# Kernel tuning notes

Measured on AMD Instinct MI355X. Metric: run time of the kernel, lower is better.

## Reference

```python
import jax, jax.numpy as jnp
import numpy as np

KERNEL_SIZE = 3
PADDING = KERNEL_SIZE // 2
EPS = 1e-12  # matches torch F.normalize default eps


def setup_inputs() -> dict:
    key = jax.random.key(0)
    k1, k2 = jax.random.split(key)
    query_feat = jax.random.normal(k1, (8, 512, 64, 64), dtype=jnp.float32)
    memory_bank = jax.random.normal(k2, (32, 512, 64, 64), dtype=jnp.float32)
    return {"query_feat": query_feat, "memory_bank": memory_bank}


def _l2_normalize(x, axis):
    n = jnp.sqrt(jnp.sum(x * x, axis=axis, keepdims=True))
    return x / jnp.maximum(n, EPS)


def reference(query_feat, memory_bank):
    # query_feat: (B, C, H, W); memory_bank: (M, C, H, W)
    b, c, h, w = query_feat.shape
    qn = _l2_normalize(query_feat, axis=1)
    mn = _l2_normalize(memory_bank, axis=1)
    # zero-pad memory spatially (matches F.unfold zero padding)
    mp = jnp.pad(mn, ((0, 0), (0, 0), (PADDING, PADDING), (PADDING, PADDING)))
    # Correlation via shifted dot-products over the K^2 window offsets,
    # keeping a running max instead of materializing (M, C, K^2, H, W).
    sim_max = None
    for di in range(KERNEL_SIZE):
        for dj in range(KERNEL_SIZE):
            shifted = mp[:, :, di:di + h, dj:dj + w]  # (M, C, H, W)
            s = jnp.einsum('mchw,bchw->bmhw', shifted, qn)  # cosine sims
            sim_max = s if sim_max is None else jnp.maximum(sim_max, s)
    pairwise = jnp.maximum(sim_max, 0.0)          # clamp(min=0), (B, M, H, W)
    group = jnp.mean(pairwise, axis=1)            # mean aggregation over M
    anomaly_map = 1.0 - group[:, None, :, :]      # (B, 1, H, W)
    return anomaly_map
```

## Files before the change

kernel.cpp:

```cpp
#include <hip/hip_runtime.h>

#define B_ 8
#define M_ 32
#define C_ 512
#define H_ 64
#define W_ 64
#define HW 4096
#define NKT 16
#define KC 32
#define TW 4
#define TH 4
#define NPOS 16
#define PW 6
#define PH 6
#define NPM 36
#define HP 66
#define WP 66
#define HPWP (HP*WP)

typedef __attribute__((ext_vector_type(8))) short short8;
typedef __attribute__((ext_vector_type(4))) float float4v;

static __device__ __forceinline__ unsigned pk_bf16(float lo, float hi) {
    unsigned r;
    asm("v_cvt_pk_bf16_f32 %0, %1, %2" : "=v"(r) : "v"(lo), "v"(hi));
    return r;
}

static __device__ __forceinline__ void load_lds16(const short* g, short* l) {
    __builtin_amdgcn_global_load_lds((const __attribute__((address_space(1))) void*)g,
                                     (__attribute__((address_space(3))) void*)l, 16, 0, 0);
}

__global__ void zero_norms(float* __restrict__ p) {
    int i = blockIdx.x * 256 + threadIdx.x;
    ((float4v*)p)[i] = (float4v){0.f, 0.f, 0.f, 0.f};
}

__global__ __launch_bounds__(512)
void prep_kernel(const float* __restrict__ Q, const float* __restrict__ Mb,
                 short* __restrict__ qT, short* __restrict__ mT,
                 float* __restrict__ nq, float* __restrict__ nm) {
    __shared__ unsigned buf[2][8704];

    const int tid = threadIdx.x;
    const bool isq = (blockIdx.x < 256);
    const int g  = isq ? (int)blockIdx.x : (int)blockIdx.x - 256;
    const int pr  = g >> 6;
    const int hq  = (g >> 2) & 15;
    const int ktg = g & 3;
    const float* base = (isq ? Q : Mb) + (size_t)(pr * 2) * C_ * HW;

    const int w4 = tid & 15, cpr = (tid >> 4) & 15, limg = tid >> 8;
    const float* lsrc = base + (size_t)limg * C_ * HW
                      + (size_t)(ktg * 128 + cpr * 2) * HW
                      + (size_t)(hq * 4) * W_ + w4 * 4;

    const int rw = tid & 63, rr2 = (tid >> 6) & 3, rim = tid >> 8;
    const unsigned* rb0 = &buf[0][(rr2 * 2 + rim) * 1088 + rw * 17];
    const unsigned* rb1 = &buf[1][(rr2 * 2 + rim) * 1088 + rw * 17];

    float4v s0 = {0.f,0.f,0.f,0.f}, s1 = s0, s2 = s0, s3 = s0;
    float4v A0, A1, A2, A3, B0, B1, B2, B3;

#define LOADP(ch) { const float* p_ = lsrc + (size_t)(ch) * 32 * HW; \
    A0 = *(const float4v*)(p_);       A1 = *(const float4v*)(p_ + 64); \
    A2 = *(const float4v*)(p_ + 128); A3 = *(const float4v*)(p_ + 192); \
    const float* q_ = p_ + HW; \
    B0 = *(const float4v*)(q_);       B1 = *(const float4v*)(q_ + 64); \
    B2 = *(const float4v*)(q_ + 128); B3 = *(const float4v*)(q_ + 192); }

#define WRITEP(bs) { unsigned* w_ = &buf[bs][limg * 1088 + cpr]; \
    s0 += A0 * A0 + B0 * B0; s1 += A1 * A1 + B1 * B1; \
    s2 += A2 * A2 + B2 * B2; s3 += A3 * A3 + B3 * B3; \
    _Pragma("unroll") \
    for (int j = 0; j < 4; ++j) { \
        w_[0 * 2176 + (w4 * 4 + j) * 17] = pk_bf16(A0[j], B0[j]); \
        w_[1 * 2176 + (w4 * 4 + j) * 17] = pk_bf16(A1[j], B1[j]); \
        w_[2 * 2176 + (w4 * 4 + j) * 17] = pk_bf16(A2[j], B2[j]); \
        w_[3 * 2176 + (w4 * 4 + j) * 17] = pk_bf16(A3[j], B3[j]); } }

#define STOREP(ch, rb) { union { unsigned u[16]; short8 v[4]; } o_; \
    _Pragma("unroll") \
    for (int q_i = 0; q_i < 16; ++q_i) o_.u[q_i] = (rb)[q_i]; \
    short* d_; \
    if (isq) d_ = qT + (((size_t)(ktg * 4 + (ch)) * HW + (size_t)(hq * 4 + rr2) * 64 + rw) * B_ \
                        + pr * 2 + rim) * KC; \
    else     d_ = mT + (((size_t)(ktg * 4 + (ch)) * HPWP + (size_t)(hq * 4 + rr2 + 1) * WP + rw + 1) * M_ \
                        + pr * 2 + rim) * KC; \
    *(short8*)(d_)      = o_.v[0]; *(short8*)(d_ + 8)  = o_.v[1]; \
    *(short8*)(d_ + 16) = o_.v[2]; *(short8*)(d_ + 24) = o_.v[3]; }

    LOADP(0); WRITEP(0); __syncthreads();
    LOADP(1); STOREP(0, rb0); WRITEP(1); __syncthreads();
    LOADP(2); STOREP(1, rb1); WRITEP(0); __syncthreads();
    LOADP(3); STOREP(2, rb0); WRITEP(1); __syncthreads();
    STOREP(3, rb1);

    float* redf = (float*)&buf[0][0];
    *(float4v*)&redf[(((cpr * 2 + limg) * 4 + 0) * 16 + w4) * 4] = s0;
    *(float4v*)&redf[(((cpr * 2 + limg) * 4 + 1) * 16 + w4) * 4] = s1;
    *(float4v*)&redf[(((cpr * 2 + limg) * 4 + 2) * 16 + w4) * 4] = s2;
    *(float4v*)&redf[(((cpr * 2 + limg) * 4 + 3) * 16 + w4) * 4] = s3;
    __syncthreads();
    {
        float t = 0.f;
        #pragma unroll
        for (int cp = 0; cp < 16; ++cp)
            t += redf[(((cp * 2 + rim) * 4 + rr2) * 16 + (rw >> 2)) * 4 + (rw & 3)];
        atomicAdd(&(isq ? nq : nm)[(size_t)(pr * 2 + rim) * HW + (size_t)(hq * 4 + rr2) * 64 + rw], t);
    }

    if (!isq) {
        short8 z = (short8){0, 0, 0, 0, 0, 0, 0, 0};
        if (tid < 256) {
            int e = tid & 7, cell = tid >> 3;
            int kk = cell & 3, rr = (cell >> 2) & 3, cs = cell >> 4;
            size_t pos2 = (size_t)(hq * 4 + 1 + rr) * WP + (cs ? 65 : 0);
            *(short8*)(mT + (((size_t)(ktg * 4 + kk) * HPWP + pos2) * M_ + pr * 2) * KC + e * 8) = z;
        }
        if (hq == 0 || hq == 15) {
            int row = (hq == 0) ? 0 : 65;
            for (int j = tid; j < 66 * 4 * 8; j += 512) {
                int e = j & 7, cell = j >> 3;
                int kk = cell & 3, col = cell >> 2;
                *(short8*)(mT + (((size_t)(ktg * 4 + kk) * HPWP + (size_t)row * WP + col) * M_ + pr * 2) * KC
                           + e * 8) = z;
            }
        }
    }
#undef LOADP
#undef WRITEP
#undef STOREP
}

__global__ __launch_bounds__(1024)
void gcm_kernel(const short* __restrict__ qT, const short* __restrict__ mT,
                const float* __restrict__ nq, const float* __restrict__ nm,
                float* __restrict__ out) {
    __shared__ __align__(16) short m_lds[NPM * M_ * KC];
    __shared__ __align__(16) short q_lds[NPOS * 16 * KC];

    const int tid = threadIdx.x;
    const int bx = blockIdx.x & 15, by = blockIdx.x >> 4;
    const int w0 = bx * TW, h0 = by * TH;
    const int wid = tid >> 6, lane = tid & 63;
    const int lw = wid & 3, lh = wid >> 2;
    const int col = lane & 15, kg = lane >> 4;
    const int mypos = lh * TW + lw;
    const int gh = h0 + lh, gw = w0 + lw;

    {
        short8 z = (short8){0, 0, 0, 0, 0, 0, 0, 0};
        *(short8*)&q_lds[tid * 8] = z;
    }

    float4v acc[9][2];
    #pragma unroll
    for (int d = 0; d < 9; ++d)
        #pragma unroll
        for (int hf = 0; hf < 2; ++hf)
            acc[d][hf] = (float4v){0.f, 0.f, 0.f, 0.f};

    for (int kt = 0; kt < NKT; ++kt) {
        __syncthreads();
        if (tid < 512) {
            int chunk = tid & 3, b = (tid >> 2) & 7, pidx = tid >> 5;
            int qh = h0 + (pidx >> 2), qw = w0 + (pidx & 3);
            const short* src = qT + (((size_t)kt * HW + qh * W_ + qw) * B_ + b) * KC + chunk * 8;
            *(short8*)&q_lds[pidx * 512 + b * KC + chunk * 8] = *(const short8*)src;
        }
        for (int j = wid; j < NPM * 2; j += 16) {
            int pm = j >> 1, half = j & 1;
            int ph = pm / PW, pw = pm % PW;
            size_t pos2 = (size_t)(h0 + ph) * WP + (w0 + pw);
            const short* gsrc = mT + ((size_t)kt * HPWP + pos2) * (M_ * KC)
                              + half * 512 + (size_t)lane * 8;
            short* ldst = m_lds + pm * 1024 + half * 512;
            load_lds16(gsrc, ldst);
        }
        __syncthreads();
        short8 aq = *(const short8*)&q_lds[mypos * 512 + col * KC + kg * 8];
        #pragma unroll
        for (int dh = 0; dh < 3; ++dh)
            #pragma unroll
            for (int dw = 0; dw < 3; ++dw) {
                const int pm = (lh + dh) * PW + (lw + dw);
                #pragma unroll
                for (int hf = 0; hf < 2; ++hf) {
                    short8 bm = *(const short8*)&m_lds[pm * 1024 + (hf * 16 + col) * KC + kg * 8];
                    acc[dh * 3 + dw][hf] =
                        __builtin_amdgcn_mfma_f32_16x16x32_bf16(aq, bm, acc[dh * 3 + dw][hf], 0, 0, 0);
                }
            }
    }

    float iq[4];
    #pragma unroll
    for (int r = 0; r < 4; ++r) {
        float ss = nq[(size_t)((kg & 1) * 4 + r) * HW + gh * W_ + gw];
        iq[r] = 1.0f / fmaxf(sqrtf(ss), 1e-12f);
    }
    float im[2][9];
    #pragma unroll
    for (int dh = 0; dh < 3; ++dh)
        #pragma unroll
        for (int dw = 0; dw < 3; ++dw) {
            int hh = min(63, max(0, gh + dh - 1));
            int ww = min(63, max(0, gw + dw - 1));
            #pragma unroll
            for (int hf = 0; hf < 2; ++hf) {
                float ss = nm[(size_t)(hf * 16 + col) * HW + hh * W_ + ww];
                im[hf][dh * 3 + dw] = 1.0f / fmaxf(sqrtf(ss), 1e-12f);
            }
        }
    float res[4];
    #pragma unroll
    for (int r = 0; r < 4; ++r) {
        float v0 = -1e30f, v1 = -1e30f;
        #pragma unroll
        for (int d = 0; d < 9; ++d) {
            v0 = fmaxf(v0, acc[d][0][r] * im[0][d]);
            v1 = fmaxf(v1, acc[d][1][r] * im[1][d]);
        }
        res[r] = fmaxf(v0 * iq[r], 0.f) + fmaxf(v1 * iq[r], 0.f);
    }
    #pragma unroll
    for (int mask = 1; mask < 16; mask <<= 1)
        #pragma unroll
        for (int r = 0; r < 4; ++r)
            res[r] += __shfl_xor(res[r], mask);

    if (col == 0 && kg < 2) {
        #pragma unroll
        for (int r = 0; r < 4; ++r) {
            int b = kg * 4 + r;
            out[(size_t)b * HW + gh * W_ + gw] = 1.0f - res[r] * (1.0f / M_);
        }
    }
}

extern "C" void kernel_launch(void* const* d_in, const int* in_sizes, int n_in,
                              void* d_out, int out_size, void* d_ws, size_t ws_size,
                              hipStream_t stream) {
    const float* Q  = (const float*)d_in[0];
    const float* Mb = (const float*)d_in[1];
    float* out = (float*)d_out;

    const size_t MT_SHORTS = (size_t)NKT * HPWP * M_ * KC;
    const size_t QT_SHORTS = (size_t)NKT * HW * B_ * KC;
    short* mT = (short*)d_ws;
    short* qT = mT + MT_SHORTS;
    float* nq = (float*)(qT + QT_SHORTS);
    float* nm = nq + B_ * HW;

    zero_norms<<<160, 256, 0, stream>>>(nq);
    prep_kernel<<<1280, 512, 0, stream>>>(Q, Mb, qT, mT, nq, nm);
    gcm_kernel<<<256, 1024, 0, stream>>>(qT, mT, nq, nm, out);
}
```

Baseline: 167.1 us.

## Remove norm-zeroing kernel via per-chunk partial norms and rework prep LDS transpose

The prep kernel now writes per-channel-group partial sums of squares to separate slots instead of atomically adding into a zeroed buffer. That removes the zero_norms launch and the atomics. The consumer kernel sums the four partials when it builds the inverse norms. The global loads are re-mapped so each thread reads 4 consecutive floats across a full row, and the LDS staging is laid out in padded slabs with 16-byte vector writes and 16-byte global stores. The cost is four times more norm reads in the gcm kernel and a larger workspace for the partial norms.

```diff
diff --git a/kernel.cpp b/kernel.cpp
--- a/kernel.cpp
+++ b/kernel.cpp
@@ -17,9 +17,12 @@
 #define HP 66
 #define WP 66
 #define HPWP (HP*WP)
+#define SLAB 1092
+#define CKS 68
 
 typedef __attribute__((ext_vector_type(8))) short short8;
 typedef __attribute__((ext_vector_type(4))) float float4v;
+typedef __attribute__((ext_vector_type(4))) unsigned uint4v;
 
 static __device__ __forceinline__ unsigned pk_bf16(float lo, float hi) {
     unsigned r;
@@ -32,16 +35,11 @@
                                      (__attribute__((address_space(3))) void*)l, 16, 0, 0);
 }
 
-__global__ void zero_norms(float* __restrict__ p) {
-    int i = blockIdx.x * 256 + threadIdx.x;
-    ((float4v*)p)[i] = (float4v){0.f, 0.f, 0.f, 0.f};
-}
-
 __global__ __launch_bounds__(512)
 void prep_kernel(const float* __restrict__ Q, const float* __restrict__ Mb,
                  short* __restrict__ qT, short* __restrict__ mT,
-                 float* __restrict__ nq, float* __restrict__ nm) {
-    __shared__ unsigned buf[2][8704];
+                 float* __restrict__ nqp, float* __restrict__ nmp) {
+    __shared__ __align__(16) unsigned buf[2][8 * SLAB];
 
     const int tid = threadIdx.x;
     const bool isq = (blockIdx.x < 256);
@@ -51,64 +49,74 @@
     const int ktg = g & 3;
     const float* base = (isq ? Q : Mb) + (size_t)(pr * 2) * C_ * HW;
 
-    const int w4 = tid & 15, cpr = (tid >> 4) & 15, limg = tid >> 8;
-    const float* lsrc = base + (size_t)limg * C_ * HW
-                      + (size_t)(ktg * 128 + cpr * 2) * HW
-                      + (size_t)(hq * 4) * W_ + w4 * 4;
-
-    const int rw = tid & 63, rr2 = (tid >> 6) & 3, rim = tid >> 8;
-    const unsigned* rb0 = &buf[0][(rr2 * 2 + rim) * 1088 + rw * 17];
-    const unsigned* rb1 = &buf[1][(rr2 * 2 + rim) * 1088 + rw * 17];
-
-    float4v s0 = {0.f,0.f,0.f,0.f}, s1 = s0, s2 = s0, s3 = s0;
-    float4v A0, A1, A2, A3, B0, B1, B2, B3;
-
-#define LOADP(ch) { const float* p_ = lsrc + (size_t)(ch) * 32 * HW; \
-    A0 = *(const float4v*)(p_);       A1 = *(const float4v*)(p_ + 64); \
-    A2 = *(const float4v*)(p_ + 128); A3 = *(const float4v*)(p_ + 192); \
-    const float* q_ = p_ + HW; \
-    B0 = *(const float4v*)(q_);       B1 = *(const float4v*)(q_ + 64); \
-    B2 = *(const float4v*)(q_ + 128); B3 = *(const float4v*)(q_ + 192); }
-
-#define WRITEP(bs) { unsigned* w_ = &buf[bs][limg * 1088 + cpr]; \
-    s0 += A0 * A0 + B0 * B0; s1 += A1 * A1 + B1 * B1; \
-    s2 += A2 * A2 + B2 * B2; s3 += A3 * A3 + B3 * B3; \
+    const int lw = tid & 63;
+    const int w4 = lw & 15, lrow = lw >> 4;
+    const int cpair = tid >> 6;
+    const float* lsrc0 = base + (size_t)(ktg * 128 + cpair * 2) * HW + hq * 4 * W_ + lw * 4;
+
+    const int sckq = tid & 3, sim = (tid >> 2) & 1, srw = tid >> 3;
+
+    float4v ssq0 = {0.f,0.f,0.f,0.f}, ssq1 = ssq0;
+    float4v V000, V001, V010, V011, V100, V101, V110, V111;
+
+#define LOADP(ch) { const float* p_ = lsrc0 + (size_t)(ch) * 32 * HW; \
+    V000 = *(const float4v*)(p_);                         V001 = *(const float4v*)(p_ + HW); \
+    V010 = *(const float4v*)(p_ + 16 * HW);               V011 = *(const float4v*)(p_ + 17 * HW); \
+    const float* q_ = p_ + (size_t)C_ * HW; \
+    V100 = *(const float4v*)(q_);                         V101 = *(const float4v*)(q_ + HW); \
+    V110 = *(const float4v*)(q_ + 16 * HW);               V111 = *(const float4v*)(q_ + 17 * HW); }
+
+#define WRITEP(bs) { \
+    ssq0 += V000 * V000 + V001 * V001 + V010 * V010 + V011 * V011; \
+    ssq1 += V100 * V100 + V101 * V101 + V110 * V110 + V111 * V111; \
+    uint4v t0, t1, t2, t3; \
     _Pragma("unroll") \
     for (int j = 0; j < 4; ++j) { \
-        w_[0 * 2176 + (w4 * 4 + j) * 17] = pk_bf16(A0[j], B0[j]); \
-        w_[1 * 2176 + (w4 * 4 + j) * 17] = pk_bf16(A1[j], B1[j]); \
-        w_[2 * 2176 + (w4 * 4 + j) * 17] = pk_bf16(A2[j], B2[j]); \
-        w_[3 * 2176 + (w4 * 4 + j) * 17] = pk_bf16(A3[j], B3[j]); } }
-
-#define STOREP(ch, rb) { union { unsigned u[16]; short8 v[4]; } o_; \
+        t0[j] = pk_bf16(V000[j], V001[j]); t1[j] = pk_bf16(V010[j], V011[j]); \
+        t2[j] = pk_bf16(V100[j], V101[j]); t3[j] = pk_bf16(V110[j], V111[j]); } \
+    unsigned* b_ = &buf[bs][0]; \
+    *(uint4v*)&b_[(lrow * 2 + 0) * SLAB + (cpair    ) * CKS + w4 * 4] = t0; \
+    *(uint4v*)&b_[(lrow * 2 + 0) * SLAB + (cpair + 8) * CKS + w4 * 4] = t1; \
+    *(uint4v*)&b_[(lrow * 2 + 1) * SLAB + (cpair    ) * CKS + w4 * 4] = t2; \
+    *(uint4v*)&b_[(lrow * 2 + 1) * SLAB + (cpair + 8) * CKS + w4 * 4] = t3; }
+
+#define STOREP(ch, bs) { \
     _Pragma("unroll") \
-    for (int q_i = 0; q_i < 16; ++q_i) o_.u[q_i] = (rb)[q_i]; \
-    short* d_; \
-    if (isq) d_ = qT + (((size_t)(ktg * 4 + (ch)) * HW + (size_t)(hq * 4 + rr2) * 64 + rw) * B_ \
-                        + pr * 2 + rim) * KC; \
-    else     d_ = mT + (((size_t)(ktg * 4 + (ch)) * HPWP + (size_t)(hq * 4 + rr2 + 1) * WP + rw + 1) * M_ \
-                        + pr * 2 + rim) * KC; \
-    *(short8*)(d_)      = o_.v[0]; *(short8*)(d_ + 8)  = o_.v[1]; \
-    *(short8*)(d_ + 16) = o_.v[2]; *(short8*)(d_ + 24) = o_.v[3]; }
+    for (int srow = 0; srow < 4; ++srow) { \
+        const unsigned* rp = &buf[bs][(srow * 2 + sim) * SLAB + srw]; \
+        union { unsigned u[4]; short8 s; } o_; \
+        _Pragma("unroll") \
+        for (int j = 0; j < 4; ++j) o_.u[j] = rp[(sckq * 4 + j) * CKS]; \
+        short* d_; \
+        if (isq) d_ = qT + (((size_t)(ktg * 4 + (ch)) * HW + (size_t)(hq * 4 + srow) * 64 + srw) * B_ \
+                            + pr * 2 + sim) * KC + sckq * 8; \
+        else     d_ = mT + (((size_t)(ktg * 4 + (ch)) * HPWP + (size_t)(hq * 4 + srow + 1) * WP + srw + 1) * M_ \
+                            + pr * 2 + sim) * KC + sckq * 8; \
+        *(short8*)d_ = o_.s; } }
 
     LOADP(0); WRITEP(0); __syncthreads();
-    LOADP(1); STOREP(0, rb0); WRITEP(1); __syncthreads();
-    LOADP(2); STOREP(1, rb1); WRITEP(0); __syncthreads();
-    LOADP(3); STOREP(2, rb0); WRITEP(1); __syncthreads();
-    STOREP(3, rb1);
-
-    float* redf = (float*)&buf[0][0];
-    *(float4v*)&redf[(((cpr * 2 + limg) * 4 + 0) * 16 + w4) * 4] = s0;
-    *(float4v*)&redf[(((cpr * 2 + limg) * 4 + 1) * 16 + w4) * 4] = s1;
-    *(float4v*)&redf[(((cpr * 2 + limg) * 4 + 2) * 16 + w4) * 4] = s2;
-    *(float4v*)&redf[(((cpr * 2 + limg) * 4 + 3) * 16 + w4) * 4] = s3;
+    LOADP(1); STOREP(0, 0); WRITEP(1); __syncthreads();
+    LOADP(2); STOREP(1, 1); WRITEP(0); __syncthreads();
+    LOADP(3); STOREP(2, 0); WRITEP(1); __syncthreads();
+    {
+        float* redf = (float*)&buf[0][0];
+        *(float4v*)&redf[(((cpair * 2 + 0) * 4 + lrow) * 16 + w4) * 4] = ssq0;
+        *(float4v*)&redf[(((cpair * 2 + 1) * 4 + lrow) * 16 + w4) * 4] = ssq1;
+    }
+    STOREP(3, 1);
     __syncthreads();
+
     {
+        const float* redf = (const float*)&buf[0][0];
+        const int rim2 = tid >> 8, rrow = (tid >> 6) & 3, rw_ = tid & 63;
         float t = 0.f;
         #pragma unroll
-        for (int cp = 0; cp < 16; ++cp)
-            t += redf[(((cp * 2 + rim) * 4 + rr2) * 16 + (rw >> 2)) * 4 + (rw & 3)];
-        atomicAdd(&(isq ? nq : nm)[(size_t)(pr * 2 + rim) * HW + (size_t)(hq * 4 + rr2) * 64 + rw], t);
+        for (int cp = 0; cp < 8; ++cp)
+            t += redf[(((cp * 2 + rim2) * 4 + rrow) * 16 + (rw_ >> 2)) * 4 + (rw_ & 3)];
+        const int img = pr * 2 + rim2;
+        const int pix = (hq * 4 + rrow) * 64 + rw_;
+        if (isq) nqp[((size_t)ktg * B_ + img) * HW + pix] = t;
+        else     nmp[((size_t)ktg * M_ + img) * HW + pix] = t;
     }
 
     if (!isq) {
@@ -136,7 +144,7 @@
 
 __global__ __launch_bounds__(1024)
 void gcm_kernel(const short* __restrict__ qT, const short* __restrict__ mT,
-                const float* __restrict__ nq, const float* __restrict__ nm,
+                const float* __restrict__ nqp, const float* __restrict__ nmp,
                 float* __restrict__ out) {
     __shared__ __align__(16) short m_lds[NPM * M_ * KC];
     __shared__ __align__(16) short q_lds[NPOS * 16 * KC];
@@ -198,7 +206,11 @@
     float iq[4];
     #pragma unroll
     for (int r = 0; r < 4; ++r) {
-        float ss = nq[(size_t)((kg & 1) * 4 + r) * HW + gh * W_ + gw];
+        int b = (kg & 1) * 4 + r;
+        float ss = 0.f;
+        #pragma unroll
+        for (int k = 0; k < 4; ++k)
+            ss += nqp[((size_t)k * B_ + b) * HW + gh * W_ + gw];
         iq[r] = 1.0f / fmaxf(sqrtf(ss), 1e-12f);
     }
     float im[2][9];
@@ -210,7 +222,11 @@
             int ww = min(63, max(0, gw + dw - 1));
             #pragma unroll
             for (int hf = 0; hf < 2; ++hf) {
-                float ss = nm[(size_t)(hf * 16 + col) * HW + hh * W_ + ww];
+                int mi = hf * 16 + col;
+                float ss = 0.f;
+                #pragma unroll
+                for (int k = 0; k < 4; ++k)
+                    ss += nmp[((size_t)k * M_ + mi) * HW + hh * W_ + ww];
                 im[hf][dh * 3 + dw] = 1.0f / fmaxf(sqrtf(ss), 1e-12f);
             }
         }
@@ -251,10 +267,9 @@
     const size_t QT_SHORTS = (size_t)NKT * HW * B_ * KC;
     short* mT = (short*)d_ws;
     short* qT = mT + MT_SHORTS;
-    float* nq = (float*)(qT + QT_SHORTS);
-    float* nm = nq + B_ * HW;
-
-    zero_norms<<<160, 256, 0, stream>>>(nq);
-    prep_kernel<<<1280, 512, 0, stream>>>(Q, Mb, qT, mT, nq, nm);
-    gcm_kernel<<<256, 1024, 0, stream>>>(qT, mT, nq, nm, out);
-}
+    float* nqp = (float*)(qT + QT_SHORTS);
+    float* nmp = nqp + 4 * B_ * HW;
+
+    prep_kernel<<<1280, 512, 0, stream>>>(Q, Mb, qT, mT, nqp, nmp);
+    gcm_kernel<<<256, 1024, 0, stream>>>(qT, mT, nqp, nmp, out);
+}
```

After: 182.5 us. 1.09x slower.

## Reorder bf16 workspace layout to image-major and restructure prep transpose

Applied to the files above, without the earlier changes.

The packed bf16 workspaces for query and memory move from position-major interleaved layouts to an image-major [img][kt][pos][KC] layout. The prep kernel is rewritten so each block handles one image, k-tile and half-image: it loads contiguous float4 rows, packs them through double-buffered LDS and writes 64-byte records, with norms reduced per chunk via atomics. The main kernel now gathers memory tiles from 32 separate image strides instead of one contiguous 1KB block per position. The intent is to make the prep kernel's global reads and writes more coalesced, at the cost of more scattered 64-byte loads in the main correlation kernel.

```diff
diff --git a/kernel.cpp b/kernel.cpp
--- a/kernel.cpp
+++ b/kernel.cpp
@@ -16,10 +16,11 @@
 #define NPM 36
 #define HP 66
 #define WP 66
-#define HPWP (HP*WP)
+#define HPWP 4356
 
 typedef __attribute__((ext_vector_type(8))) short short8;
 typedef __attribute__((ext_vector_type(4))) float float4v;
+typedef __attribute__((ext_vector_type(4))) unsigned uint4v;
 
 static __device__ __forceinline__ unsigned pk_bf16(float lo, float hi) {
     unsigned r;
@@ -41,97 +42,83 @@
 void prep_kernel(const float* __restrict__ Q, const float* __restrict__ Mb,
                  short* __restrict__ qT, short* __restrict__ mT,
                  float* __restrict__ nq, float* __restrict__ nm) {
-    __shared__ unsigned buf[2][8704];
+    __shared__ unsigned bufu[2][4096];
+    __shared__ float    redf[2][2048];
 
     const int tid = threadIdx.x;
-    const bool isq = (blockIdx.x < 256);
-    const int g  = isq ? (int)blockIdx.x : (int)blockIdx.x - 256;
-    const int pr  = g >> 6;
-    const int hq  = (g >> 2) & 15;
-    const int ktg = g & 3;
-    const float* base = (isq ? Q : Mb) + (size_t)(pr * 2) * C_ * HW;
-
-    const int w4 = tid & 15, cpr = (tid >> 4) & 15, limg = tid >> 8;
-    const float* lsrc = base + (size_t)limg * C_ * HW
-                      + (size_t)(ktg * 128 + cpr * 2) * HW
-                      + (size_t)(hq * 4) * W_ + w4 * 4;
-
-    const int rw = tid & 63, rr2 = (tid >> 6) & 3, rim = tid >> 8;
-    const unsigned* rb0 = &buf[0][(rr2 * 2 + rim) * 1088 + rw * 17];
-    const unsigned* rb1 = &buf[1][(rr2 * 2 + rim) * 1088 + rw * 17];
-
-    float4v s0 = {0.f,0.f,0.f,0.f}, s1 = s0, s2 = s0, s3 = s0;
-    float4v A0, A1, A2, A3, B0, B1, B2, B3;
-
-#define LOADP(ch) { const float* p_ = lsrc + (size_t)(ch) * 32 * HW; \
-    A0 = *(const float4v*)(p_);       A1 = *(const float4v*)(p_ + 64); \
-    A2 = *(const float4v*)(p_ + 128); A3 = *(const float4v*)(p_ + 192); \
-    const float* q_ = p_ + HW; \
-    B0 = *(const float4v*)(q_);       B1 = *(const float4v*)(q_ + 64); \
-    B2 = *(const float4v*)(q_ + 128); B3 = *(const float4v*)(q_ + 192); }
-
-#define WRITEP(bs) { unsigned* w_ = &buf[bs][limg * 1088 + cpr]; \
-    s0 += A0 * A0 + B0 * B0; s1 += A1 * A1 + B1 * B1; \
-    s2 += A2 * A2 + B2 * B2; s3 += A3 * A3 + B3 * B3; \
+    const int ii = blockIdx.x >> 5;
+    const int kt = (blockIdx.x >> 1) & 15;
+    const int ph = blockIdx.x & 1;
+    const bool isq = (ii < B_);
+    const int mi = ii - B_;
+    const float* base = isq ? Q + (size_t)ii * C_ * HW : Mb + (size_t)mi * C_ * HW;
+
+    const int l = tid & 63, w = tid >> 6;
+    const float* lsrc = base + (size_t)(kt * 32 + 4 * w) * HW + ph * 2048 + l * 4;
+    float* nrm = (isq ? nq + (size_t)ii * HW : nm + (size_t)mi * HW) + ph * 2048;
+
+    float4v V0, V1, V2, V3;
+
+#define LOADC(cc) { const float* p_ = lsrc + (cc) * 256; \
+    V0 = *(const float4v*)(p_); \
+    V1 = *(const float4v*)(p_ + HW); \
+    V2 = *(const float4v*)(p_ + 2 * HW); \
+    V3 = *(const float4v*)(p_ + 3 * HW); }
+
+#define PACKW(bs) { \
+    float4v s_ = V0 * V0 + V1 * V1 + V2 * V2 + V3 * V3; \
+    uint4v a_, b_; \
     _Pragma("unroll") \
-    for (int j = 0; j < 4; ++j) { \
-        w_[0 * 2176 + (w4 * 4 + j) * 17] = pk_bf16(A0[j], B0[j]); \
-        w_[1 * 2176 + (w4 * 4 + j) * 17] = pk_bf16(A1[j], B1[j]); \
-        w_[2 * 2176 + (w4 * 4 + j) * 17] = pk_bf16(A2[j], B2[j]); \
-        w_[3 * 2176 + (w4 * 4 + j) * 17] = pk_bf16(A3[j], B3[j]); } }
-
-#define STOREP(ch, rb) { union { unsigned u[16]; short8 v[4]; } o_; \
+    for (int j = 0; j < 4; ++j) { a_[j] = pk_bf16(V0[j], V1[j]); b_[j] = pk_bf16(V2[j], V3[j]); } \
+    *(uint4v*)&bufu[bs][(2 * w    ) * 256 + l * 4] = a_; \
+    *(uint4v*)&bufu[bs][(2 * w + 1) * 256 + l * 4] = b_; \
+    *(float4v*)&redf[bs][w * 256 + l * 4] = s_; }
+
+#define GATHERST(cc, bs) { \
     _Pragma("unroll") \
-    for (int q_i = 0; q_i < 16; ++q_i) o_.u[q_i] = (rb)[q_i]; \
-    short* d_; \
-    if (isq) d_ = qT + (((size_t)(ktg * 4 + (ch)) * HW + (size_t)(hq * 4 + rr2) * 64 + rw) * B_ \
-                        + pr * 2 + rim) * KC; \
-    else     d_ = mT + (((size_t)(ktg * 4 + (ch)) * HPWP + (size_t)(hq * 4 + rr2 + 1) * WP + rw + 1) * M_ \
-                        + pr * 2 + rim) * KC; \
-    *(short8*)(d_)      = o_.v[0]; *(short8*)(d_ + 8)  = o_.v[1]; \
-    *(short8*)(d_ + 16) = o_.v[2]; *(short8*)(d_ + 24) = o_.v[3]; }
-
-    LOADP(0); WRITEP(0); __syncthreads();
-    LOADP(1); STOREP(0, rb0); WRITEP(1); __syncthreads();
-    LOADP(2); STOREP(1, rb1); WRITEP(0); __syncthreads();
-    LOADP(3); STOREP(2, rb0); WRITEP(1); __syncthreads();
-    STOREP(3, rb1);
-
-    float* redf = (float*)&buf[0][0];
-    *(float4v*)&redf[(((cpr * 2 + limg) * 4 + 0) * 16 + w4) * 4] = s0;
-    *(float4v*)&redf[(((cpr * 2 + limg) * 4 + 1) * 16 + w4) * 4] = s1;
-    *(float4v*)&redf[(((cpr * 2 + limg) * 4 + 2) * 16 + w4) * 4] = s2;
-    *(float4v*)&redf[(((cpr * 2 + limg) * 4 + 3) * 16 + w4) * 4] = s3;
-    __syncthreads();
-    {
-        float t = 0.f;
-        #pragma unroll
-        for (int cp = 0; cp < 16; ++cp)
-            t += redf[(((cp * 2 + rim) * 4 + rr2) * 16 + (rw >> 2)) * 4 + (rw & 3)];
-        atomicAdd(&(isq ? nq : nm)[(size_t)(pr * 2 + rim) * HW + (size_t)(hq * 4 + rr2) * 64 + rw], t);
-    }
+    for (int it = 0; it < 2; ++it) { \
+        int t_ = tid + it * 512; int rec = t_ >> 2, quad = t_ & 3; \
+        union { unsigned u[4]; short8 s; } o_; \
+        _Pragma("unroll") \
+        for (int i = 0; i < 4; ++i) o_.u[i] = bufu[bs][(quad * 4 + i) * 256 + rec]; \
+        int pos = ph * 2048 + (cc) * 256 + rec; \
+        short* d_; \
+        if (isq) d_ = qT + ((size_t)(ii * NKT + kt) * HW + pos) * KC + quad * 8; \
+        else { int hh = pos >> 6, wc = pos & 63; \
+               d_ = mT + ((size_t)(mi * NKT + kt) * HPWP + (size_t)(hh + 1) * WP + wc + 1) * KC + quad * 8; } \
+        *(short8*)d_ = o_.s; } \
+    if (tid < 256) { \
+        float t_ = 0.f; \
+        _Pragma("unroll") \
+        for (int w2 = 0; w2 < 8; ++w2) t_ += redf[bs][w2 * 256 + tid]; \
+        atomicAdd(nrm + (cc) * 256 + tid, t_); } }
+
+    LOADC(0); PACKW(0); __syncthreads();
+    #pragma unroll
+    for (int cc = 0; cc < 8; ++cc) {
+        if (cc < 7) LOADC(cc + 1);
+        GATHERST(cc, cc & 1);
+        if (cc < 7) PACKW((cc + 1) & 1);
+        __syncthreads();
+    }
+#undef LOADC
+#undef PACKW
+#undef GATHERST
 
     if (!isq) {
         short8 z = (short8){0, 0, 0, 0, 0, 0, 0, 0};
-        if (tid < 256) {
-            int e = tid & 7, cell = tid >> 3;
-            int kk = cell & 3, rr = (cell >> 2) & 3, cs = cell >> 4;
-            size_t pos2 = (size_t)(hq * 4 + 1 + rr) * WP + (cs ? 65 : 0);
-            *(short8*)(mT + (((size_t)(ktg * 4 + kk) * HPWP + pos2) * M_ + pr * 2) * KC + e * 8) = z;
-        }
-        if (hq == 0 || hq == 15) {
-            int row = (hq == 0) ? 0 : 65;
-            for (int j = tid; j < 66 * 4 * 8; j += 512) {
-                int e = j & 7, cell = j >> 3;
-                int kk = cell & 3, col = cell >> 2;
-                *(short8*)(mT + (((size_t)(ktg * 4 + kk) * HPWP + (size_t)row * WP + col) * M_ + pr * 2) * KC
-                           + e * 8) = z;
+        for (int j = tid; j < 130 * 4; j += 512) {
+            int cell = j >> 2, piece = j & 3;
+            int pos2;
+            if (cell < 66) pos2 = ph ? (65 * WP + cell) : cell;
+            else {
+                int k = cell - 66;
+                int row = (ph ? 33 : 1) + (k >> 1);
+                pos2 = row * WP + ((k & 1) ? 65 : 0);
             }
-        }
-    }
-#undef LOADP
-#undef WRITEP
-#undef STOREP
+            *(short8*)(mT + ((size_t)(mi * NKT + kt) * HPWP + pos2) * KC + piece * 8) = z;
+        }
+    }
 }
 
 __global__ __launch_bounds__(1024)
@@ -150,6 +137,10 @@
     const int mypos = lh * TW + lw;
     const int gh = h0 + lh, gw = w0 + lw;
 
+    const size_t MSTRIDE = (size_t)NKT * HPWP * KC;
+    const size_t moff0 = (size_t)(lane >> 2) * MSTRIDE + (lane & 3) * 8;
+    const size_t moff1 = moff0 + 16 * MSTRIDE;
+
     {
         short8 z = (short8){0, 0, 0, 0, 0, 0, 0, 0};
         *(short8*)&q_lds[tid * 8] = z;
@@ -167,15 +158,14 @@
         if (tid < 512) {
             int chunk = tid & 3, b = (tid >> 2) & 7, pidx = tid >> 5;
             int qh = h0 + (pidx >> 2), qw = w0 + (pidx & 3);
-            const short* src = qT + (((size_t)kt * HW + qh * W_ + qw) * B_ + b) * KC + chunk * 8;
+            const short* src = qT + ((size_t)(b * NKT + kt) * HW + qh * W_ + qw) * KC + chunk * 8;
             *(short8*)&q_lds[pidx * 512 + b * KC + chunk * 8] = *(const short8*)src;
         }
         for (int j = wid; j < NPM * 2; j += 16) {
             int pm = j >> 1, half = j & 1;
-            int ph = pm / PW, pw = pm % PW;
-            size_t pos2 = (size_t)(h0 + ph) * WP + (w0 + pw);
-            const short* gsrc = mT + ((size_t)kt * HPWP + pos2) * (M_ * KC)
-                              + half * 512 + (size_t)lane * 8;
+            int ph_ = pm / PW, pw_ = pm % PW;
+            size_t pos2 = (size_t)(h0 + ph_) * WP + (w0 + pw_);
+            const short* gsrc = mT + ((size_t)kt * HPWP + pos2) * KC + (half ? moff1 : moff0);
             short* ldst = m_lds + pm * 1024 + half * 512;
             load_lds16(gsrc, ldst);
         }
@@ -247,8 +237,8 @@
     const float* Mb = (const float*)d_in[1];
     float* out = (float*)d_out;
 
-    const size_t MT_SHORTS = (size_t)NKT * HPWP * M_ * KC;
-    const size_t QT_SHORTS = (size_t)NKT * HW * B_ * KC;
+    const size_t MT_SHORTS = (size_t)M_ * NKT * HPWP * KC;
+    const size_t QT_SHORTS = (size_t)B_ * NKT * HW * KC;
     short* mT = (short*)d_ws;
     short* qT = mT + MT_SHORTS;
     float* nq = (float*)(qT + QT_SHORTS);
```

After: 183.3 us. 9.7% more time.
